# Performance work log

Hardware: AMD Instinct MI355X
Metric: run time of the kernel (lower is better)

Reference implementation:

```python
import jax, jax.numpy as jnp
import numpy as np

H, W, T = 720, 1280, 20
B, N = 8, 500000


def setup_inputs() -> dict:
    key = jax.random.key(0)
    kx, ky, kt, kp, kc = jax.random.split(key, 5)
    x = jnp.floor(jax.random.uniform(kx, (B, N)) * W)          # pixel x in [0, W)
    y = jnp.floor(jax.random.uniform(ky, (B, N)) * H)          # pixel y in [0, H)
    t = jax.random.uniform(kt, (B, N))                          # normalized time in [0, 1]
    p = jax.random.bernoulli(kp, 0.5, (B, N)).astype(jnp.float32)  # polarity {0,1}
    eventBlock = jnp.stack([x, y, t, p], axis=-1).astype(jnp.float32)  # (B, N, 4)
    eventCounts = jax.random.randint(kc, (B,), N // 2, N + 1).astype(jnp.int64)
    return {"eventBlock": eventBlock, "eventCounts": eventCounts}


def reference(eventBlock, eventCounts):
    # events -> (B, W, H, T) voxel grid via temporal bilinear scatter-add,
    # then permute(0,3,2,1) -> (B, T, H, W) as in EV2VoxelGrid.forward
    x = eventBlock[..., 0].astype(jnp.int32)                    # (B, N)
    y = eventBlock[..., 1].astype(jnp.int32)
    t = eventBlock[..., 2]
    pol = eventBlock[..., 3] * 2.0 - 1.0                        # {0,1} -> {-1,+1}

    valid = jnp.arange(N)[None, :] < eventCounts[:, None]       # (B, N) mask by counts

    tb = t * (T - 1)                                            # continuous bin coord
    k0 = jnp.floor(tb).astype(jnp.int32)
    w1 = tb - k0.astype(tb.dtype)
    w0 = 1.0 - w1
    k0c = jnp.clip(k0, 0, T - 1)
    k1c = jnp.clip(k0 + 1, 0, T - 1)

    xc = jnp.clip(x, 0, W - 1)
    yc = jnp.clip(y, 0, H - 1)
    b = jnp.arange(B, dtype=jnp.int32)[:, None]                 # (B, 1)
    base = ((b * W + xc) * H + yc) * T                          # flat (b, x, y) offset

    v0 = jnp.where(valid, pol * w0, 0.0)
    v1 = jnp.where(valid, pol * w1, 0.0)

    grid = jnp.zeros((B * W * H * T,), dtype=eventBlock.dtype)
    grid = grid.at[(base + k0c).ravel()].add(v0.ravel())
    grid = grid.at[(base + k1c).ravel()].add(v1.ravel())
    grid = grid.reshape(B, W, H, T)
    return jnp.transpose(grid, (0, 3, 2, 1))                    # (B, T, H, W)
```

## Files before the change

kernel.cpp:

```cpp
#include <hip/hip_runtime.h>

#define GH 720
#define GW 1280
#define GT 20
#define GB 8
#define NEV 500000
#define TOTAL (GB * NEV)

#define CY 90
#define NCOARSE (GB * CY)
#define CAPC 6144
#define PAD 32
#define EVB 8192
#define NBLK1 ((TOTAL + EVB - 1) / EVB)

#define TY 8
#define TX 64
#define NTXB (GW / TX)
#define OVF_CAP (1u << 20)

typedef float vfloat4 __attribute__((ext_vector_type(4)));


__global__ __launch_bounds__(256) void k_zero(unsigned* __restrict__ gcnt)
{
    int i = blockIdx.x * blockDim.x + threadIdx.x;
    if (i < NCOARSE * PAD + 1) gcnt[i] = 0u;
}

__global__ __launch_bounds__(256) void k_part(
    const float4* __restrict__ ev, const int* __restrict__ counts,
    unsigned* __restrict__ gcnt, unsigned* __restrict__ buckets,
    uint2* __restrict__ ovf)
{
    __shared__ unsigned hist[NCOARSE];
    __shared__ unsigned lbase[NCOARSE];
    __shared__ unsigned hist2[NCOARSE];
    const int tid = threadIdx.x;
    const int base = blockIdx.x * EVB + tid;

    for (int c = tid; c < NCOARSE; c += 256) { hist[c] = 0u; hist2[c] = 0u; }
    __syncthreads();

    for (int j = 0; j < EVB / 256; j++) {
        int i = base + j * 256;
        if (i >= TOTAL) break;
        int b = i / NEV;
        int n = i - b * NEV;
        if (n >= counts[b]) continue;
        float4 e = ev[i];
        int y = min(max((int)e.y, 0), GH - 1);
        atomicAdd(&hist[b * CY + (y >> 3)], 1u);
    }
    __syncthreads();

    for (int c = tid; c < NCOARSE; c += 256) {
        unsigned h = hist[c];
        lbase[c] = h ? atomicAdd(&gcnt[c * PAD], h) : 0u;
    }
    __syncthreads();

    for (int j = 0; j < EVB / 256; j++) {
        int i = base + j * 256;
        if (i >= TOTAL) break;
        int b = i / NEV;
        int n = i - b * NEV;
        if (n >= counts[b]) continue;
        float4 e = ev[i];
        int x = min(max((int)e.x, 0), GW - 1);
        int y = min(max((int)e.y, 0), GH - 1);
        int c = b * CY + (y >> 3);

        float tb = e.z * (float)(GT - 1);
        int k0 = (int)floorf(tb);
        float w1 = tb - (float)k0;
        int k0c = min(max(k0, 0), GT - 1);
        unsigned p = (e.w > 0.5f) ? 1u : 0u;

        unsigned pos = lbase[c] + atomicAdd(&hist2[c], 1u);
        if (pos < CAPC) {
            unsigned w1q = __float2uint_rn(w1 * 4095.0f);
            unsigned rec = (unsigned)x | ((unsigned)(y & 7) << 11) | (p << 14)
                         | ((unsigned)k0c << 15) | (w1q << 20);
            buckets[(size_t)c * CAPC + pos] = rec;
        } else {
            unsigned word0 = (unsigned)x | ((unsigned)y << 11) | (p << 21)
                           | ((unsigned)k0c << 22) | ((unsigned)b << 27);
            unsigned o = atomicAdd(&gcnt[NCOARSE * PAD], 1u);
            if (o < OVF_CAP) ovf[o] = make_uint2(word0, __float_as_uint(w1));
        }
    }
}

__global__ __launch_bounds__(256) void k_faccum(
    const unsigned* __restrict__ buckets, const unsigned* __restrict__ gcnt,
    float* __restrict__ out)
{
    __shared__ float tile[GT * TY * TX];
    const int c  = blockIdx.x / NTXB;
    const int tx = blockIdx.x % NTXB;
    const int tid = threadIdx.x;

    vfloat4* t4 = (vfloat4*)tile;
    for (int j = tid; j < GT * TY * (TX / 4); j += 256)
        t4[j] = (vfloat4){0.f, 0.f, 0.f, 0.f};
    __syncthreads();

    unsigned m = min(gcnt[c * PAD], (unsigned)CAPC);
    const unsigned* bp = buckets + (size_t)c * CAPC;
    for (unsigned idx = tid; idx < m; idx += 256) {
        unsigned r = bp[idx];
        if ((int)((r & 2047u) >> 6) != tx) continue;
        int xx = r & 63;
        int yy = (r >> 11) & 7;
        float pol = ((r >> 14) & 1u) ? 1.0f : -1.0f;
        int k0 = (r >> 15) & 31;
        float w1 = (float)(r >> 20) * (1.0f / 4095.0f);
        int k1 = min(k0 + 1, GT - 1);
        atomicAdd(&tile[(k0 * TY + yy) * TX + xx], pol * (1.0f - w1));
        atomicAdd(&tile[(k1 * TY + yy) * TX + xx], pol * w1);
    }
    __syncthreads();

    const int b  = c / CY;
    const int y0 = (c % CY) * TY;
    vfloat4* o4 = (vfloat4*)out;
    for (int j = tid; j < GT * TY * (TX / 4); j += 256) {
        int row = j >> 4;
        int col = j & 15;
        int k  = row >> 3;
        int yy = row & 7;
        int off = ((b * GT + k) * GH + (y0 + yy)) * (GW / 4) + tx * (TX / 4) + col;
        __builtin_nontemporal_store(t4[j], &o4[off]);
    }
}

__global__ __launch_bounds__(256) void k_overflow(
    const uint2* __restrict__ ovf, const unsigned* __restrict__ gcnt,
    float* __restrict__ out)
{
    unsigned n = min(gcnt[NCOARSE * PAD], OVF_CAP);
    for (unsigned i = blockIdx.x * blockDim.x + threadIdx.x; i < n;
         i += gridDim.x * blockDim.x) {
        uint2 r = ovf[i];
        int x  = r.x & 2047;
        int y  = (r.x >> 11) & 1023;
        int p  = (r.x >> 21) & 1;
        int k0 = (r.x >> 22) & 31;
        int b  = (r.x >> 27) & 7;
        float w1 = __uint_as_float(r.y);
        float w0 = 1.0f - w1;
        float pol = p ? 1.0f : -1.0f;
        int k1 = min(k0 + 1, GT - 1);
        atomicAdd(&out[((b * GT + k0) * GH + y) * GW + x], pol * w0);
        atomicAdd(&out[((b * GT + k1) * GH + y) * GW + x], pol * w1);
    }
}

__global__ __launch_bounds__(256) void ev2voxel_scatter(
    const float4* __restrict__ ev, const int* __restrict__ counts,
    float* __restrict__ out)
{
    int i = blockIdx.x * blockDim.x + threadIdx.x;
    if (i >= TOTAL) return;
    int b = i / NEV;
    int n = i - b * NEV;
    if (n >= counts[b]) return;
    float4 e = ev[i];
    int x = min(max((int)e.x, 0), GW - 1);
    int y = min(max((int)e.y, 0), GH - 1);
    float pol = e.w * 2.0f - 1.0f;
    float tb = e.z * (float)(GT - 1);
    int k0 = (int)floorf(tb);
    float w1 = tb - (float)k0;
    float w0 = 1.0f - w1;
    int k0c = min(max(k0, 0), GT - 1);
    int k1c = min(max(k0 + 1, 0), GT - 1);
    int rowbase = (b * GT) * GH;
    atomicAdd(&out[(rowbase + k0c * GH + y) * GW + x], pol * w0);
    atomicAdd(&out[(rowbase + k1c * GH + y) * GW + x], pol * w1);
}

extern "C" void kernel_launch(void* const* d_in, const int* in_sizes, int n_in,
                              void* d_out, int out_size, void* d_ws, size_t ws_size,
                              hipStream_t stream) {
    const float4* ev = (const float4*)d_in[0];
    const int* counts = (const int*)d_in[1];
    float* out = (float*)d_out;

    const size_t gcnt_off   = 0;
    const size_t bucket_off = (size_t)NCOARSE * PAD + PAD;
    size_t ovf_off          = bucket_off + (size_t)NCOARSE * CAPC;
    if (ovf_off & 1) ovf_off++;
    const size_t need_bytes = (ovf_off + (size_t)OVF_CAP * 2) * 4;

    if (ws_size < need_bytes) {
        (void)hipMemsetAsync(out, 0, (size_t)out_size * sizeof(float), stream);
        ev2voxel_scatter<<<(TOTAL + 255) / 256, 256, 0, stream>>>(ev, counts, out);
        return;
    }

    unsigned* ws = (unsigned*)d_ws;
    unsigned* gcnt    = ws + gcnt_off;
    unsigned* buckets = ws + bucket_off;
    uint2*    ovf     = (uint2*)(ws + ovf_off);

    k_zero<<<(NCOARSE * PAD + 1 + 255) / 256, 256, 0, stream>>>(gcnt);
    k_part<<<NBLK1, 256, 0, stream>>>(ev, counts, gcnt, buckets, ovf);
    k_faccum<<<NCOARSE * NTXB, 256, 0, stream>>>(buckets, gcnt, out);
    k_overflow<<<64, 256, 0, stream>>>(ovf, gcnt, out);
}
```

Baseline: 194.9 us.

## Stage partitioned records in LDS and write buckets contiguously

The partition kernel now computes a block-local prefix sum over the coarse-bin histogram and places each packed event record into an LDS stash sorted by bin. A second pass then writes the stash out in order, using a binary search to find each record's bin, so global bucket stores become contiguous runs instead of scattered single-word writes. This adds a 32KB LDS stash, a 256-step scan with many barriers, and a per-element binary search. The extra LDS use may reduce occupancy. Overflow records are rebuilt from the quantized weight, so they lose some precision compared with the old float weight.

```diff
diff --git a/kernel.cpp b/kernel.cpp
--- a/kernel.cpp
+++ b/kernel.cpp
@@ -13,6 +13,7 @@
 #define PAD 32
 #define EVB 8192
 #define NBLK1 ((TOTAL + EVB - 1) / EVB)
+#define CHUNKC ((NCOARSE + 255) / 256)
 
 #define TY 8
 #define TX 64
@@ -33,13 +34,15 @@
     unsigned* __restrict__ gcnt, unsigned* __restrict__ buckets,
     uint2* __restrict__ ovf)
 {
+    __shared__ unsigned stash[EVB];
     __shared__ unsigned hist[NCOARSE];
+    __shared__ unsigned foff[NCOARSE + 1];
     __shared__ unsigned lbase[NCOARSE];
-    __shared__ unsigned hist2[NCOARSE];
+    __shared__ unsigned ssum[256];
     const int tid = threadIdx.x;
     const int base = blockIdx.x * EVB + tid;
 
-    for (int c = tid; c < NCOARSE; c += 256) { hist[c] = 0u; hist2[c] = 0u; }
+    for (int c = tid; c < NCOARSE; c += 256) hist[c] = 0u;
     __syncthreads();
 
     for (int j = 0; j < EVB / 256; j++) {
@@ -58,6 +61,24 @@
         unsigned h = hist[c];
         lbase[c] = h ? atomicAdd(&gcnt[c * PAD], h) : 0u;
     }
+
+    int lo = tid * CHUNKC, hi = min(lo + CHUNKC, NCOARSE);
+    unsigned s = 0;
+    for (int j = lo; j < hi; j++) s += hist[j];
+    ssum[tid] = s;
+    __syncthreads();
+    for (int off = 1; off < 256; off <<= 1) {
+        unsigned v = (tid >= off) ? ssum[tid - off] : 0u;
+        __syncthreads();
+        ssum[tid] += v;
+        __syncthreads();
+    }
+    unsigned bse = (tid > 0) ? ssum[tid - 1] : 0u;
+    for (int j = lo; j < hi; j++) { foff[j] = bse; bse += hist[j]; }
+    if (tid == 255) foff[NCOARSE] = bse;
+    __syncthreads();
+
+    for (int c = tid; c < NCOARSE; c += 256) hist[c] = 0u;
     __syncthreads();
 
     for (int j = 0; j < EVB / 256; j++) {
@@ -76,16 +97,32 @@
         float w1 = tb - (float)k0;
         int k0c = min(max(k0, 0), GT - 1);
         unsigned p = (e.w > 0.5f) ? 1u : 0u;
-
-        unsigned pos = lbase[c] + atomicAdd(&hist2[c], 1u);
-        if (pos < CAPC) {
-            unsigned w1q = __float2uint_rn(w1 * 4095.0f);
-            unsigned rec = (unsigned)x | ((unsigned)(y & 7) << 11) | (p << 14)
-                         | ((unsigned)k0c << 15) | (w1q << 20);
-            buckets[(size_t)c * CAPC + pos] = rec;
+        unsigned w1q = __float2uint_rn(w1 * 4095.0f);
+        unsigned rec = (unsigned)x | ((unsigned)(y & 7) << 11) | (p << 14)
+                     | ((unsigned)k0c << 15) | (w1q << 20);
+        unsigned rk = atomicAdd(&hist[c], 1u);
+        stash[foff[c] + rk] = rec;
+    }
+    __syncthreads();
+
+    unsigned vcount = foff[NCOARSE];
+    for (unsigned j = tid; j < vcount; j += 256) {
+        int lo2 = 0, hi2 = NCOARSE;
+        while (hi2 - lo2 > 1) {
+            int mid = (lo2 + hi2) >> 1;
+            if (foff[mid] <= j) lo2 = mid; else hi2 = mid;
+        }
+        unsigned c = (unsigned)lo2;
+        unsigned r = stash[j];
+        unsigned dst = lbase[c] + (j - foff[c]);
+        if (dst < CAPC) {
+            buckets[(size_t)c * CAPC + dst] = r;
         } else {
-            unsigned word0 = (unsigned)x | ((unsigned)y << 11) | (p << 21)
-                           | ((unsigned)k0c << 22) | ((unsigned)b << 27);
+            int b = c / CY;
+            int y = (c % CY) * 8 + ((r >> 11) & 7);
+            unsigned word0 = (r & 2047u) | ((unsigned)y << 11) | (((r >> 14) & 1u) << 21)
+                           | (((r >> 15) & 31u) << 22) | ((unsigned)b << 27);
+            float w1 = (float)(r >> 20) * (1.0f / 4095.0f);
             unsigned o = atomicAdd(&gcnt[NCOARSE * PAD], 1u);
             if (o < OVF_CAP) ovf[o] = make_uint2(word0, __float_as_uint(w1));
         }
```

Measured after the change: 217.8 us. 11.7% more time.

## Add second-level bucketing pass so accumulate blocks read only their own events

Applied to the files above, without the earlier changes.

Before, each of the 20 x-tile blocks per coarse bucket scanned the whole coarse bucket of up to 6144 records and discarded those outside its tile, so every record was read 20 times. A new k_mid kernel splits each coarse bucket into per-x-tile fine buckets of capacity 512, and k_accum then reads only its own fine bucket. This removes the redundant global reads and filtering. It costs an extra kernel launch, an extra write and read of all records, more workspace, and a second overflow path for fine buckets that exceed capacity.

```diff
diff --git a/kernel.cpp b/kernel.cpp
--- a/kernel.cpp
+++ b/kernel.cpp
@@ -17,15 +17,21 @@
 #define TY 8
 #define TX 64
 #define NTXB (GW / TX)
+#define NFINE (NCOARSE * NTXB)
+#define CAPF 512
+#define MCHUNK 1024
+#define NCH (CAPC / MCHUNK)
 #define OVF_CAP (1u << 20)
 
 typedef float vfloat4 __attribute__((ext_vector_type(4)));
 
 
-__global__ __launch_bounds__(256) void k_zero(unsigned* __restrict__ gcnt)
+__global__ __launch_bounds__(256) void k_zero(unsigned* __restrict__ gcnt,
+                                              unsigned* __restrict__ fcnt)
 {
     int i = blockIdx.x * blockDim.x + threadIdx.x;
     if (i < NCOARSE * PAD + 1) gcnt[i] = 0u;
+    if (i < NFINE) fcnt[i] = 0u;
 }
 
 __global__ __launch_bounds__(256) void k_part(
@@ -92,13 +98,62 @@
     }
 }
 
-__global__ __launch_bounds__(256) void k_faccum(
-    const unsigned* __restrict__ buckets, const unsigned* __restrict__ gcnt,
+__global__ __launch_bounds__(256) void k_mid(
+    const unsigned* __restrict__ buckets, unsigned* __restrict__ gcnt,
+    unsigned* __restrict__ fcnt, unsigned* __restrict__ buckets2,
+    uint2* __restrict__ ovf)
+{
+    __shared__ unsigned stash[MCHUNK];
+    __shared__ unsigned fh[NTXB], fbase[NTXB], fh2[NTXB];
+    const int c = blockIdx.x / NCH;
+    const int chunk = blockIdx.x % NCH;
+    const int tid = threadIdx.x;
+
+    unsigned m = min(gcnt[c * PAD], (unsigned)CAPC);
+    unsigned lo = chunk * MCHUNK;
+    if (lo >= m) return;
+    unsigned cnt = min(m - lo, (unsigned)MCHUNK);
+
+    if (tid < NTXB) { fh[tid] = 0u; fh2[tid] = 0u; }
+    __syncthreads();
+
+    const unsigned* bp = buckets + (size_t)c * CAPC + lo;
+    for (unsigned i = tid; i < cnt; i += 256) {
+        unsigned r = bp[i];
+        stash[i] = r;
+        atomicAdd(&fh[(r & 2047u) >> 6], 1u);
+    }
+    __syncthreads();
+
+    if (tid < NTXB && fh[tid])
+        fbase[tid] = atomicAdd(&fcnt[c * NTXB + tid], fh[tid]);
+    __syncthreads();
+
+    for (unsigned i = tid; i < cnt; i += 256) {
+        unsigned r = stash[i];
+        unsigned tx = (r & 2047u) >> 6;
+        unsigned dst = fbase[tx] + atomicAdd(&fh2[tx], 1u);
+        if (dst < CAPF) {
+            buckets2[(size_t)(c * NTXB + tx) * CAPF + dst] = r;
+        } else {
+            int b = c / CY;
+            int y = (c % CY) * 8 + ((r >> 11) & 7);
+            unsigned word0 = (r & 2047u) | ((unsigned)y << 11)
+                           | (((r >> 14) & 1u) << 21)
+                           | (((r >> 15) & 31u) << 22) | ((unsigned)b << 27);
+            float w1 = (float)(r >> 20) * (1.0f / 4095.0f);
+            unsigned o = atomicAdd(&gcnt[NCOARSE * PAD], 1u);
+            if (o < OVF_CAP) ovf[o] = make_uint2(word0, __float_as_uint(w1));
+        }
+    }
+}
+
+__global__ __launch_bounds__(256) void k_accum(
+    const unsigned* __restrict__ buckets2, const unsigned* __restrict__ fcnt,
     float* __restrict__ out)
 {
     __shared__ float tile[GT * TY * TX];
-    const int c  = blockIdx.x / NTXB;
-    const int tx = blockIdx.x % NTXB;
+    const int f = blockIdx.x;
     const int tid = threadIdx.x;
 
     vfloat4* t4 = (vfloat4*)tile;
@@ -106,11 +161,10 @@
         t4[j] = (vfloat4){0.f, 0.f, 0.f, 0.f};
     __syncthreads();
 
-    unsigned m = min(gcnt[c * PAD], (unsigned)CAPC);
-    const unsigned* bp = buckets + (size_t)c * CAPC;
+    unsigned m = min(fcnt[f], (unsigned)CAPF);
+    const unsigned* bp = buckets2 + (size_t)f * CAPF;
     for (unsigned idx = tid; idx < m; idx += 256) {
         unsigned r = bp[idx];
-        if ((int)((r & 2047u) >> 6) != tx) continue;
         int xx = r & 63;
         int yy = (r >> 11) & 7;
         float pol = ((r >> 14) & 1u) ? 1.0f : -1.0f;
@@ -122,6 +176,8 @@
     }
     __syncthreads();
 
+    const int c  = f / NTXB;
+    const int tx = f % NTXB;
     const int b  = c / CY;
     const int y0 = (c % CY) * TY;
     vfloat4* o4 = (vfloat4*)out;
@@ -188,9 +244,11 @@
     const int* counts = (const int*)d_in[1];
     float* out = (float*)d_out;
 
-    const size_t gcnt_off   = 0;
-    const size_t bucket_off = (size_t)NCOARSE * PAD + PAD;
-    size_t ovf_off          = bucket_off + (size_t)NCOARSE * CAPC;
+    const size_t gcnt_off    = 0;
+    const size_t fcnt_off    = (size_t)NCOARSE * PAD + PAD;
+    const size_t bucket_off  = fcnt_off + NFINE;
+    const size_t bucket2_off = bucket_off + (size_t)NCOARSE * CAPC;
+    size_t ovf_off           = bucket2_off + (size_t)NFINE * CAPF;
     if (ovf_off & 1) ovf_off++;
     const size_t need_bytes = (ovf_off + (size_t)OVF_CAP * 2) * 4;
 
@@ -201,12 +259,15 @@
     }
 
     unsigned* ws = (unsigned*)d_ws;
-    unsigned* gcnt    = ws + gcnt_off;
-    unsigned* buckets = ws + bucket_off;
-    uint2*    ovf     = (uint2*)(ws + ovf_off);
-
-    k_zero<<<(NCOARSE * PAD + 1 + 255) / 256, 256, 0, stream>>>(gcnt);
+    unsigned* gcnt     = ws + gcnt_off;
+    unsigned* fcnt     = ws + fcnt_off;
+    unsigned* buckets  = ws + bucket_off;
+    unsigned* buckets2 = ws + bucket2_off;
+    uint2*    ovf      = (uint2*)(ws + ovf_off);
+
+    k_zero<<<(NCOARSE * PAD + 1 + 255) / 256, 256, 0, stream>>>(gcnt, fcnt);
     k_part<<<NBLK1, 256, 0, stream>>>(ev, counts, gcnt, buckets, ovf);
-    k_faccum<<<NCOARSE * NTXB, 256, 0, stream>>>(buckets, gcnt, out);
+    k_mid<<<NCOARSE * NCH, 256, 0, stream>>>(buckets, gcnt, fcnt, buckets2, ovf);
+    k_accum<<<NFINE, 256, 0, stream>>>(buckets2, fcnt, out);
     k_overflow<<<64, 256, 0, stream>>>(ovf, gcnt, out);
 }
```

Measured after the change: 185.9 us. 4.6% less time.
